# Kernel tuning notes

Measured on AMD Instinct MI355X. Metric: run time of the kernel, lower is better.

The kernel has to match this reference:

```python
import jax, jax.numpy as jnp
import numpy as np

# Config from init_kwargs
B = 16
CIN = 128
COUT = 256
N = 16        # num_filters
L = 32        # length
K = 3         # kernel_size
KAPPA = 4
STRIDE = 1
PAD = 2
LP = L + PAD  # padded spatial length for FFT


def make_wn():
    # DFT-derived channel-mixing matrix, (cin, d) with d = cout // n
    v = np.arange(CIN)[:, None]
    sr = N * CIN // COUT
    inds = np.arange(CIN)[np.arange(CIN) % sr == 0]
    M = v @ v[inds].T  # (cin, d)
    wn = np.exp((2j * np.pi / CIN) * M) / CIN
    return jnp.asarray(wn.astype(np.complex64))


def setup_inputs() -> dict:
    key = jax.random.key(0)
    k1, k2 = jax.random.split(key)
    x = jax.random.normal(k1, (B, CIN, L, L), dtype=jnp.float32)
    rng = float(np.sqrt(KAPPA / (CIN * K * K)))
    weight = (jax.random.uniform(k2, (N, CIN // KAPPA, K, K), dtype=jnp.float32) - 0.5) * 2.0 * rng
    return {"x": x, "weight": weight}


def reference(x, weight):
    wn = make_wn()  # complex64 (CIN, COUT//N), constant buffer
    # 3D real FFT over (channel, h, w); weight zero-padded from cin//kappa -> cin channels
    x_hat = jnp.fft.rfftn(x, s=(CIN, LP, LP), axes=(-3, -2, -1))          # (B, CIN, LP, LP//2+1)
    w_hat = jnp.fft.rfftn(weight, s=(CIN, LP, LP), axes=(-3, -2, -1))     # (N, CIN, LP, LP//2+1)
    freq = jnp.einsum('bchw,nchw->bnchw', x_hat, w_hat)                   # broadcast, no reduction
    out = jnp.fft.irfftn(freq, s=(LP, LP), axes=(-2, -1))                 # real (B, N, CIN, LP, LP)
    # complex channel mix contracting c -> d; result complex, take real part
    out = jnp.einsum('cd,bnchw->bndhw', wn, out)                          # (B, N, D, LP, LP) complex
    out = out.real[:, :, :, PAD:, PAD:]                                   # (B, N, D, L, L)
    out = jnp.transpose(out, (0, 2, 1, 3, 4))                             # (B, D, N, L, L)
    out = out.reshape(out.shape[0], -1, out.shape[3], out.shape[4])       # (B, COUT, L, L)
    if STRIDE == 2:
        idx = jnp.arange(0, L, 2)
        out = out[:, :, idx, :][:, :, :, idx]
    return out
```

## Files before the change

kernel.cpp:

```cpp
#include <hip/hip_runtime.h>
#include <hip/hip_bf16.h>


typedef __attribute__((ext_vector_type(8))) short short8;
typedef __attribute__((ext_vector_type(4))) float floatx4;

#define NT 512
#define LCH 168
#define SROWS 34
#define XSROW (SROWS * LCH)

template<int D, bool DUP>
__device__ __forceinline__ void compute_d(const char* basep, const short8 af[9],
                                          float* opbase) {
    floatx4 a0 = {0.f,0.f,0.f,0.f}, a1 = {0.f,0.f,0.f,0.f};
    floatx4 b0 = {0.f,0.f,0.f,0.f}, b1 = {0.f,0.f,0.f,0.f};
#pragma unroll
    for (int u = 0; u < 3; ++u)
#pragma unroll
        for (int v = 0; v < 3; ++v) {
            const int t = u * 3 + v;
            const short8 ba = *(const short8*)(basep +
                ((u * SROWS + v) * LCH + 8 * (8 + D)) * 2);
            if (t & 1) a1 = __builtin_amdgcn_mfma_f32_16x16x32_bf16(af[t], ba, a1, 0, 0, 0);
            else       a0 = __builtin_amdgcn_mfma_f32_16x16x32_bf16(af[t], ba, a0, 0, 0, 0);
            if (!DUP) {
                const short8 bb = *(const short8*)(basep +
                    ((u * SROWS + v) * LCH + 8 * (8 - D)) * 2);
                if (t & 1) b1 = __builtin_amdgcn_mfma_f32_16x16x32_bf16(af[t], bb, b1, 0, 0, 0);
                else       b0 = __builtin_amdgcn_mfma_f32_16x16x32_bf16(af[t], bb, b0, 0, 0, 0);
            }
        }
    floatx4 acc = a0 + a1;
    if (DUP) acc = acc + acc;
    else     acc = acc + (b0 + b1);
    float* op = opbase + D * 16384;
    __builtin_nontemporal_store(acc.x, op);
    __builtin_nontemporal_store(acc.y, op + 1024);
    __builtin_nontemporal_store(acc.z, op + 2048);
    __builtin_nontemporal_store(acc.w, op + 3072);
    if (D >= 1 && D <= 7) {
        float* op2 = opbase + (16 - D) * 16384;
        __builtin_nontemporal_store(acc.x, op2);
        __builtin_nontemporal_store(acc.y, op2 + 1024);
        __builtin_nontemporal_store(acc.z, op2 + 2048);
        __builtin_nontemporal_store(acc.w, op2 + 3072);
    }
}

__global__ __launch_bounds__(NT, 4)
void fconv_mfma(const float* __restrict__ x,
                const float* __restrict__ wgt,
                float* __restrict__ out) {
    __shared__ __align__(16) short xs[3 * XSROW];
    __shared__ __align__(16) short wf[9 * 640];

    const int bid = blockIdx.x;
    const int b   = (bid & 7) + (((bid >> 3) & 1) << 3);
    const int r   = bid >> 4;
    const int tid  = threadIdx.x;
    const int lane = tid & 63;
    const int wv   = tid >> 6;

    {
        const int nn = tid >> 5;
        const int c2 = tid & 31;
        const float* wb = wgt + (size_t)(nn * 32 + c2) * 9;
        const int pos = nn * 40 + (c2 & 24) + (7 - (c2 & 7));
#pragma unroll
        for (int k = 0; k < 9; ++k) {
            __hip_bfloat16 h = __float2bfloat16(0.5f * wb[k]);
            wf[(8 - k) * 640 + pos] = __builtin_bit_cast(short, h);
        }
    }

    const float* xb_base = x + ((size_t)b << 17);
#pragma unroll
    for (int it = 0; it < 4; ++it) {
        const int idx = it * NT + tid;
        if (idx < 1920) {
            const int col  = idx & 31;
            const int rest = idx >> 5;
            const int oL   = rest / 3;
            const int lrow = rest - oL * 3;
            const int grow = r + lrow;
            short8 g;
            if (grow < 32) {
                float v[8];
#pragma unroll
                for (int j = 0; j < 8; ++j) {
                    const int m = (oL * 8 + j - 95) & 127;
                    v[j] = xb_base[((m << 5) + grow) * 32 + col];
                }
                union { __hip_bfloat162 h2[4]; short8 s8; } u;
#pragma unroll
                for (int p = 0; p < 4; ++p)
                    u.h2[p] = __float22bfloat162_rn(make_float2(v[2 * p], v[2 * p + 1]));
                g = u.s8;
            } else {
                g = short8{0, 0, 0, 0, 0, 0, 0, 0};
            }
            *(short8*)&xs[(lrow * SROWS + col) * LCH + oL * 8] = g;
        }
    }
    if (tid < 120) {
        const int oL   = tid % 20;
        const int rem  = tid / 20;
        const int lrow = rem >> 1;
        const int col  = 32 + (rem & 1);
        short8 z = {0, 0, 0, 0, 0, 0, 0, 0};
        *(short8*)&xs[(lrow * SROWS + col) * LCH + oL * 8] = z;
    }

    __syncthreads();

    const int n = lane & 15;
    const int q = lane >> 4;
    short8 af[9];
#pragma unroll
    for (int t = 0; t < 9; ++t)
        af[t] = *(const short8*)&wf[t * 640 + n * 40 + q * 8];

#pragma unroll
    for (int i = 0; i < 2; ++i) {
        const int s0 = i << 4;
        const char* basep = (const char*)xs + ((s0 + n) * LCH + 8 * (3 - q)) * 2;
        float* opbase = out + ((size_t)((b * 256 + q * 4) * 32 + r) << 5) + s0 + n;
        switch (wv) {
        case 0: compute_d<0, true >(basep, af, opbase);
                compute_d<8, true >(basep, af, opbase); break;
        case 1: compute_d<4, false>(basep, af, opbase); break;
        case 2: compute_d<2, false>(basep, af, opbase); break;
        case 3: compute_d<6, false>(basep, af, opbase); break;
        case 4: compute_d<1, false>(basep, af, opbase); break;
        case 5: compute_d<5, false>(basep, af, opbase); break;
        case 6: compute_d<3, false>(basep, af, opbase); break;
        default: compute_d<7, false>(basep, af, opbase); break;
        }
    }
}

extern "C" void kernel_launch(void* const* d_in, const int* in_sizes, int n_in,
                              void* d_out, int out_size, void* d_ws, size_t ws_size,
                              hipStream_t stream) {
    const float* x   = (const float*)d_in[0];
    const float* wgt = (const float*)d_in[1];
    float* out = (float*)d_out;
    (void)in_sizes; (void)n_in; (void)out_size; (void)d_ws; (void)ws_size;

    fconv_mfma<<<dim3(512), dim3(NT), 0, stream>>>(x, wgt, out);
}
```

Before: 68.17 us.

## Compute two output rows per block and stage results through LDS for coalesced stores

Each block now handles two output rows instead of one, so the x halo rows loaded into shared memory are reused across both rows and the grid is halved to 256 blocks. Accumulators are written into a 64KB shared buffer aliased over the input tiles, then stored to global memory as contiguous float4 nontemporal stores instead of scattered scalar stores. Input loads are also marked nontemporal. The cost is more shared memory and registers per block, lower occupancy (launch bounds 2) and fewer blocks than CUs on a 256-CU part, plus an extra barrier and LDS round trip.

Result: slower. 69.79 us (+2.4%).

```diff
diff --git a/kernel.cpp b/kernel.cpp
--- a/kernel.cpp
+++ b/kernel.cpp
@@ -11,8 +11,7 @@
 #define XSROW (SROWS * LCH)
 
 template<int D, bool DUP>
-__device__ __forceinline__ void compute_d(const char* basep, const short8 af[9],
-                                          float* opbase) {
+__device__ __forceinline__ floatx4 compute_d_acc(const char* basep, const short8 af[9]) {
     floatx4 a0 = {0.f,0.f,0.f,0.f}, a1 = {0.f,0.f,0.f,0.f};
     floatx4 b0 = {0.f,0.f,0.f,0.f}, b1 = {0.f,0.f,0.f,0.f};
 #pragma unroll
@@ -34,30 +33,21 @@
     floatx4 acc = a0 + a1;
     if (DUP) acc = acc + acc;
     else     acc = acc + (b0 + b1);
-    float* op = opbase + D * 16384;
-    __builtin_nontemporal_store(acc.x, op);
-    __builtin_nontemporal_store(acc.y, op + 1024);
-    __builtin_nontemporal_store(acc.z, op + 2048);
-    __builtin_nontemporal_store(acc.w, op + 3072);
-    if (D >= 1 && D <= 7) {
-        float* op2 = opbase + (16 - D) * 16384;
-        __builtin_nontemporal_store(acc.x, op2);
-        __builtin_nontemporal_store(acc.y, op2 + 1024);
-        __builtin_nontemporal_store(acc.z, op2 + 2048);
-        __builtin_nontemporal_store(acc.w, op2 + 3072);
-    }
+    return acc;
 }
 
-__global__ __launch_bounds__(NT, 4)
+__global__ __launch_bounds__(NT, 2)
 void fconv_mfma(const float* __restrict__ x,
                 const float* __restrict__ wgt,
                 float* __restrict__ out) {
-    __shared__ __align__(16) short xs[3 * XSROW];
-    __shared__ __align__(16) short wf[9 * 640];
+    __shared__ __align__(16) char smem[65536];
+    short* xs = (short*)smem;
+    short* wf = (short*)(smem + 46080);
+    float* ot = (float*)smem;
 
     const int bid = blockIdx.x;
     const int b   = (bid & 7) + (((bid >> 3) & 1) << 3);
-    const int r   = bid >> 4;
+    const int r0  = (bid >> 4) * 2;
     const int tid  = threadIdx.x;
     const int lane = tid & 63;
     const int wv   = tid >> 6;
@@ -76,34 +66,33 @@
 
     const float* xb_base = x + ((size_t)b << 17);
 #pragma unroll
-    for (int it = 0; it < 4; ++it) {
-        const int idx = it * NT + tid;
-        if (idx < 1920) {
-            const int col  = idx & 31;
-            const int rest = idx >> 5;
-            const int oL   = rest / 3;
-            const int lrow = rest - oL * 3;
-            const int grow = r + lrow;
-            short8 g;
-            if (grow < 32) {
-                float v[8];
-#pragma unroll
-                for (int j = 0; j < 8; ++j) {
-                    const int m = (oL * 8 + j - 95) & 127;
-                    v[j] = xb_base[((m << 5) + grow) * 32 + col];
-                }
-                union { __hip_bfloat162 h2[4]; short8 s8; } u;
-#pragma unroll
-                for (int p = 0; p < 4; ++p)
-                    u.h2[p] = __float22bfloat162_rn(make_float2(v[2 * p], v[2 * p + 1]));
-                g = u.s8;
-            } else {
-                g = short8{0, 0, 0, 0, 0, 0, 0, 0};
+    for (int it = 0; it < 5; ++it) {
+        const int idx  = wv * 320 + it * 64 + lane;
+        const int col  = idx & 31;
+        const int rest = idx >> 5;
+        const int lrow = rest & 3;
+        const int oL   = rest >> 2;
+        const int grow = r0 + lrow;
+        short8 g;
+        if (grow < 32) {
+            float v[8];
+#pragma unroll
+            for (int j = 0; j < 8; ++j) {
+                const int m = (oL * 8 + j - 95) & 127;
+                v[j] = __builtin_nontemporal_load(
+                    xb_base + ((m << 5) + grow) * 32 + col);
             }
-            *(short8*)&xs[(lrow * SROWS + col) * LCH + oL * 8] = g;
-        }
-    }
-    if (tid < 120) {
+            union { __hip_bfloat162 h2[4]; short8 s8; } u;
+#pragma unroll
+            for (int p = 0; p < 4; ++p)
+                u.h2[p] = __float22bfloat162_rn(make_float2(v[2 * p], v[2 * p + 1]));
+            g = u.s8;
+        } else {
+            g = short8{0, 0, 0, 0, 0, 0, 0, 0};
+        }
+        *(short8*)&xs[(lrow * SROWS + col) * LCH + oL * 8] = g;
+    }
+    if (tid < 160) {
         const int oL   = tid % 20;
         const int rem  = tid / 20;
         const int lrow = rem >> 1;
@@ -121,22 +110,97 @@
     for (int t = 0; t < 9; ++t)
         af[t] = *(const short8*)&wf[t * 640 + n * 40 + q * 8];
 
-#pragma unroll
-    for (int i = 0; i < 2; ++i) {
-        const int s0 = i << 4;
-        const char* basep = (const char*)xs + ((s0 + n) * LCH + 8 * (3 - q)) * 2;
-        float* opbase = out + ((size_t)((b * 256 + q * 4) * 32 + r) << 5) + s0 + n;
-        switch (wv) {
-        case 0: compute_d<0, true >(basep, af, opbase);
-                compute_d<8, true >(basep, af, opbase); break;
-        case 1: compute_d<4, false>(basep, af, opbase); break;
-        case 2: compute_d<2, false>(basep, af, opbase); break;
-        case 3: compute_d<6, false>(basep, af, opbase); break;
-        case 4: compute_d<1, false>(basep, af, opbase); break;
-        case 5: compute_d<5, false>(basep, af, opbase); break;
-        case 6: compute_d<3, false>(basep, af, opbase); break;
-        default: compute_d<7, false>(basep, af, opbase); break;
-        }
+    const char* xb0 = (const char*)xs;
+#define BP(lr, s0) (xb0 + (((lr) * SROWS + (s0) + n) * LCH + 8 * (3 - q)) * 2)
+    floatx4 rA[4];
+    floatx4 rB[4];
+    int dA, dB = -1;
+    switch (wv) {
+    case 0:
+        rA[0] = compute_d_acc<0, true >(BP(0, 0), af);
+        rA[1] = compute_d_acc<0, true >(BP(0, 16), af);
+        rA[2] = compute_d_acc<0, true >(BP(1, 0), af);
+        rA[3] = compute_d_acc<0, true >(BP(1, 16), af);
+        rB[0] = compute_d_acc<8, true >(BP(0, 0), af);
+        rB[1] = compute_d_acc<8, true >(BP(0, 16), af);
+        rB[2] = compute_d_acc<8, true >(BP(1, 0), af);
+        rB[3] = compute_d_acc<8, true >(BP(1, 16), af);
+        dA = 0; dB = 8; break;
+    case 1:
+        rA[0] = compute_d_acc<4, false>(BP(0, 0), af);
+        rA[1] = compute_d_acc<4, false>(BP(0, 16), af);
+        rA[2] = compute_d_acc<4, false>(BP(1, 0), af);
+        rA[3] = compute_d_acc<4, false>(BP(1, 16), af);
+        dA = 4; break;
+    case 2:
+        rA[0] = compute_d_acc<2, false>(BP(0, 0), af);
+        rA[1] = compute_d_acc<2, false>(BP(0, 16), af);
+        rA[2] = compute_d_acc<2, false>(BP(1, 0), af);
+        rA[3] = compute_d_acc<2, false>(BP(1, 16), af);
+        dA = 2; break;
+    case 3:
+        rA[0] = compute_d_acc<6, false>(BP(0, 0), af);
+        rA[1] = compute_d_acc<6, false>(BP(0, 16), af);
+        rA[2] = compute_d_acc<6, false>(BP(1, 0), af);
+        rA[3] = compute_d_acc<6, false>(BP(1, 16), af);
+        dA = 6; break;
+    case 4:
+        rA[0] = compute_d_acc<1, false>(BP(0, 0), af);
+        rA[1] = compute_d_acc<1, false>(BP(0, 16), af);
+        rA[2] = compute_d_acc<1, false>(BP(1, 0), af);
+        rA[3] = compute_d_acc<1, false>(BP(1, 16), af);
+        dA = 1; break;
+    case 5:
+        rA[0] = compute_d_acc<5, false>(BP(0, 0), af);
+        rA[1] = compute_d_acc<5, false>(BP(0, 16), af);
+        rA[2] = compute_d_acc<5, false>(BP(1, 0), af);
+        rA[3] = compute_d_acc<5, false>(BP(1, 16), af);
+        dA = 5; break;
+    case 6:
+        rA[0] = compute_d_acc<3, false>(BP(0, 0), af);
+        rA[1] = compute_d_acc<3, false>(BP(0, 16), af);
+        rA[2] = compute_d_acc<3, false>(BP(1, 0), af);
+        rA[3] = compute_d_acc<3, false>(BP(1, 16), af);
+        dA = 3; break;
+    default:
+        rA[0] = compute_d_acc<7, false>(BP(0, 0), af);
+        rA[1] = compute_d_acc<7, false>(BP(0, 16), af);
+        rA[2] = compute_d_acc<7, false>(BP(1, 0), af);
+        rA[3] = compute_d_acc<7, false>(BP(1, 16), af);
+        dA = 7; break;
+    }
+#undef BP
+
+    __syncthreads();
+
+    {
+        const int chb = q * 4;
+#pragma unroll
+        for (int sub = 0; sub < 4; ++sub) {
+            const int lr = sub >> 1;
+            const int s  = ((sub & 1) << 4) + n;
+#pragma unroll
+            for (int reg = 0; reg < 4; ++reg) {
+                const float vA = rA[sub][reg];
+                ot[((dA * 16 + chb + reg) * 2 + lr) * 32 + s] = vA;
+                if (dA >= 1 && dA <= 7)
+                    ot[(((16 - dA) * 16 + chb + reg) * 2 + lr) * 32 + s] = vA;
+                if (dB >= 0)
+                    ot[((dB * 16 + chb + reg) * 2 + lr) * 32 + s] = rB[sub][reg];
+            }
+        }
+    }
+
+    __syncthreads();
+
+    float* ob = out + ((size_t)b << 18) + r0 * 32;
+#pragma unroll
+    for (int k = 0; k < 8; ++k) {
+        const int idx = k * 2048 + tid * 4;
+        const floatx4 v = *(const floatx4*)&ot[idx];
+        const int ch = idx >> 6;
+        const int rs = idx & 63;
+        __builtin_nontemporal_store(v, (floatx4*)(ob + ch * 1024 + rs));
     }
 }
 
@@ -148,5 +212,5 @@
     float* out = (float*)d_out;
     (void)in_sizes; (void)n_in; (void)out_size; (void)d_ws; (void)ws_size;
 
-    fconv_mfma<<<dim3(512), dim3(NT), 0, stream>>>(x, wgt, out);
+    fconv_mfma<<<dim3(256), dim3(NT), 0, stream>>>(x, wgt, out);
 }
```
